# Performance work log

Measured on AMD Instinct MI355X. Metric: run time of the kernel, lower is better.

Reference implementation:

```python
import jax, jax.numpy as jnp
import numpy as np

B, S, E = 2, 2048, 2048
H, HD = 32, 64          # n_heads, head_dim
KV, REP = 8, 4          # n_kv_head, n_kv_head_rep (H == KV*REP)
NEG = -1e9


def setup_inputs() -> dict:
    key = jax.random.key(0)
    ks = jax.random.split(key, 6)
    x = jax.random.normal(ks[0], (B, S, E), dtype=jnp.float32)
    # Llama RoPE tables: angles[p, i] = p / 10000^(2i/HD)
    inv_freq = 1.0 / (10000.0 ** (jnp.arange(0, HD, 2, dtype=jnp.float32) / HD))
    angles = jnp.arange(S, dtype=jnp.float32)[:, None] * inv_freq[None, :]  # [S, HD/2]
    cos, sin = jnp.cos(angles), jnp.sin(angles)
    # causal additive mask [S, S]
    mask = jnp.where(jnp.tril(jnp.ones((S, S), dtype=bool)), 0.0, NEG).astype(jnp.float32)
    sc = 0.02
    wq = jax.random.normal(ks[1], (E, H * HD), dtype=jnp.float32) * sc
    wk = jax.random.normal(ks[2], (E, KV * HD), dtype=jnp.float32) * sc
    wv = jax.random.normal(ks[3], (E, KV * HD), dtype=jnp.float32) * sc
    wo = jax.random.normal(ks[4], (H * HD, E), dtype=jnp.float32) * sc
    return {"x": x, "cos": cos, "sin": sin, "mask": mask,
            "wq": wq, "wk": wk, "wv": wv, "wo": wo, "start_pos": 0}


def _rope(t, cos, sin):
    # t: [B, S, h, HD]; rotate consecutive pairs (Llama complex convention)
    tp = t.reshape(t.shape[:-1] + (HD // 2, 2))
    t1, t2 = tp[..., 0], tp[..., 1]
    c = cos[None, :, None, :]
    s = sin[None, :, None, :]
    out = jnp.stack([t1 * c - t2 * s, t1 * s + t2 * c], axis=-1)
    return out.reshape(t.shape)


def reference(x, cos, sin, mask, wq, wk, wv, wo, start_pos):
    b, s, _ = x.shape
    q = (x @ wq).reshape(b, s, H, HD)
    k = (x @ wk).reshape(b, s, KV, HD)
    v = (x @ wv).reshape(b, s, KV, HD)
    q = _rope(q, cos, sin)
    k = _rope(k, cos, sin)
    # KV-cache: with start_pos=0 and full-seq prefill, the cache slice
    # [:, :start_pos+s] is exactly the freshly written k/v, so use them directly.
    # Grouped attention without materializing repeated K/V:
    # q -> [b, KV, REP, s, HD]; k,v -> [b, KV, s, HD]
    qg = q.transpose(0, 2, 1, 3).reshape(b, KV, REP, s, HD)
    kg = k.transpose(0, 2, 1, 3)
    vg = v.transpose(0, 2, 1, 3)
    scale = 1.0 / jnp.sqrt(jnp.float32(HD))
    scores = jnp.einsum('bgrqd,bgkd->bgrqk', qg, kg) * scale + mask
    attn = jax.nn.softmax(scores, axis=-1)
    og = jnp.einsum('bgrqk,bgkd->bgrqd', attn, vg)     # [b, KV, REP, s, HD]
    out = og.reshape(b, H, s, HD).transpose(0, 2, 1, 3).reshape(b, s, H * HD)
    return out @ wo
```

## Files before the change

kernel.cpp:

```cpp
#include <hip/hip_runtime.h>
#include <stdint.h>

#define S_LEN 2048
#define NTOK  4096
#define EMB   2048
#define NHEAD 32
#define HDIM  64
#define NKVH  8

typedef __bf16 bf16x8 __attribute__((ext_vector_type(8)));
typedef float  f32x4  __attribute__((ext_vector_type(4)));

#define AS1 __attribute__((address_space(1)))
#define AS3 __attribute__((address_space(3)))

#if __has_builtin(__builtin_amdgcn_exp2f)
#define EXP2(x) __builtin_amdgcn_exp2f(x)
#else
#define EXP2(x) exp2f(x)
#endif

#define QSCALE 0.1803368867f

__device__ __forceinline__ uint16_t f2bf(float f) {
  uint32_t u = __float_as_uint(f);
  u += 0x7fffu + ((u >> 16) & 1u);
  return (uint16_t)(u >> 16);
}
__device__ __forceinline__ float bf2f(uint16_t h) {
  return __uint_as_float(((uint32_t)h) << 16);
}
__device__ __forceinline__ void gld16(const void* g, void* l) {
  __builtin_amdgcn_global_load_lds((const AS1 uint32_t*)g, (AS3 uint32_t*)l, 16, 0, 0);
}
__device__ __forceinline__ f32x4 mfma16(bf16x8 a, bf16x8 b, f32x4 c) {
  return __builtin_amdgcn_mfma_f32_16x16x32_bf16(a, b, c, 0, 0, 0);
}

__global__ void k_cvt(const float* __restrict__ in, uint16_t* __restrict__ out) {
  int i = (blockIdx.x * 256 + threadIdx.x) * 4;
  float4 v = *(const float4*)(in + i);
  ushort4 o;
  o.x = f2bf(v.x); o.y = f2bf(v.y); o.z = f2bf(v.z); o.w = f2bf(v.w);
  *(ushort4*)(out + i) = o;
}

__global__ void k_transpose(const float* __restrict__ in, uint16_t* __restrict__ out,
                            int R, int C) {
  __shared__ float tile[32][33];
  int c0 = blockIdx.x * 32, r0 = blockIdx.y * 32;
  int tx = threadIdx.x & 31, ty = threadIdx.x >> 5;
#pragma unroll
  for (int j = 0; j < 32; j += 8)
    tile[ty + j][tx] = in[(size_t)(r0 + ty + j) * C + c0 + tx];
  __syncthreads();
#pragma unroll
  for (int j = 0; j < 32; j += 8)
    out[(size_t)(c0 + ty + j) * R + r0 + tx] = f2bf(tile[tx][ty + j]);
}

__global__ void k_transpose_v(const uint16_t* __restrict__ qkv, uint16_t* __restrict__ out) {
  __shared__ uint16_t tile[32][33];
  int s0 = blockIdx.x * 32, hd0 = blockIdx.y * 32, bh = blockIdx.z;
  int b = bh >> 3, kvh = bh & 7;
  int tx = threadIdx.x & 31, ty = threadIdx.x >> 5;
#pragma unroll
  for (int j = 0; j < 32; j += 8)
    tile[ty + j][tx] =
        qkv[((size_t)b * S_LEN + s0 + ty + j) * 3072 + 2560 + kvh * 64 + hd0 + tx];
  __syncthreads();
#pragma unroll
  for (int j = 0; j < 32; j += 8)
    out[((size_t)bh * 64 + hd0 + ty + j) * S_LEN + s0 + tx] = tile[tx][ty + j];
}

template <int N_REP, typename OUT_T>
__global__ __launch_bounds__(512, 1) void k_gemm256(
    const uint16_t* __restrict__ A, const uint16_t* __restrict__ BT,
    OUT_T* __restrict__ C, int M, int N, int K) {
  constexpr int LDSH = 16384 + N_REP * 4096;
  __shared__ uint16_t lds[2][LDSH];
  const int tid = threadIdx.x, lane = tid & 63, w = tid >> 6;
  const int wm = w >> 2, wn = w & 3;
  const int l16 = lane & 15, lg = lane >> 4;
  const int nbn = N / (N_REP * 64);
  const int nwg = gridDim.x, cpx = nwg >> 3;
  const int swz = ((int)blockIdx.x & 7) * cpx + ((int)blockIdx.x >> 3);
  const int bm = (swz / nbn) * 256, bn = (swz % nbn) * (N_REP * 64);

  f32x4 acc[8][N_REP] = {};

  const int srow = tid >> 3, sslot = tid & 7;
  const int schunk = (sslot ^ (srow & 7)) * 8;
  const uint16_t* Ag = A + (size_t)(bm + srow) * K + schunk;
  const uint16_t* Bg = BT + (size_t)(bn + srow) * K + schunk;

  auto stageA = [&](int d, int r, int k0) {
    gld16(Ag + (size_t)r * 64 * K + k0, &lds[d][r * 4096 + tid * 8]);
  };
  auto stageB = [&](int d, int r, int k0) {
    gld16(Bg + (size_t)r * 64 * K + k0, &lds[d][16384 + r * 4096 + tid * 8]);
  };
  auto lda = [&](int d, int mf, int s) -> bf16x8 {
    int row = wm * 128 + mf * 16 + l16;
    int slot = (s * 4 + lg) ^ (row & 7);
    return *(const bf16x8*)(&lds[d][row * 64 + slot * 8]);
  };
  auto ldb = [&](int d, int nf, int s) -> bf16x8 {
    int row = wn * (N_REP * 16) + nf * 16 + l16;
    int slot = (s * 4 + lg) ^ (row & 7);
    return *(const bf16x8*)(&lds[d][16384 + row * 64 + slot * 8]);
  };

  const int NT = K >> 6;
#pragma unroll
  for (int r = 0; r < 4; ++r) stageA(0, r, 0);
#pragma unroll
  for (int r = 0; r < N_REP; ++r) stageB(0, r, 0);
#pragma unroll
  for (int r = 0; r < 4; ++r) if (1 < NT) stageA(1, r, 64);
  asm volatile("s_waitcnt vmcnt(4)" ::: "memory");
  __builtin_amdgcn_s_barrier();

  for (int kt = 0; kt < NT; ++kt) {
    const int cur = kt & 1;
    const int nk0 = (kt + 1) << 6, nnk0 = (kt + 2) << 6;
    const bool m1 = (kt + 1 < NT), m2 = (kt + 2 < NT);
    bf16x8 a[4][2], a2[4][2], b[N_REP][2];
#pragma unroll
    for (int mi = 0; mi < 4; ++mi) { a[mi][0] = lda(cur, mi, 0); a[mi][1] = lda(cur, mi, 1); }
#pragma unroll
    for (int ni = 0; ni < N_REP; ++ni) { b[ni][0] = ldb(cur, ni, 0); b[ni][1] = ldb(cur, ni, 1); }
    if (m1) {
#pragma unroll
      for (int r = 0; r < N_REP; ++r) stageB(cur ^ 1, r, nk0);
    }
    __builtin_amdgcn_s_barrier();
    asm volatile("s_waitcnt lgkmcnt(0)" ::: "memory");
    __builtin_amdgcn_sched_barrier(0);
    __builtin_amdgcn_s_setprio(1);
#pragma unroll
    for (int mi = 0; mi < 4; ++mi)
#pragma unroll
      for (int ni = 0; ni < 2; ++ni) {
        acc[mi][ni] = mfma16(a[mi][0], b[ni][0], acc[mi][ni]);
        acc[mi][ni] = mfma16(a[mi][1], b[ni][1], acc[mi][ni]);
      }
    __builtin_amdgcn_s_setprio(0);
    __builtin_amdgcn_s_barrier();
#pragma unroll
    for (int mi = 0; mi < 4; ++mi) { a2[mi][0] = lda(cur, 4 + mi, 0); a2[mi][1] = lda(cur, 4 + mi, 1); }
    __builtin_amdgcn_s_barrier();
    asm volatile("s_waitcnt lgkmcnt(0)" ::: "memory");
    __builtin_amdgcn_sched_barrier(0);
    __builtin_amdgcn_s_setprio(1);
    if constexpr (N_REP == 3) {
#pragma unroll
      for (int mi = 0; mi < 4; ++mi) {
        acc[mi][2] = mfma16(a[mi][0], b[2][0], acc[mi][2]);
        acc[mi][2] = mfma16(a[mi][1], b[2][1], acc[mi][2]);
      }
    }
#pragma unroll
    for (int mi = 0; mi < 4; ++mi) {
      acc[4 + mi][0] = mfma16(a2[mi][0], b[0][0], acc[4 + mi][0]);
      acc[4 + mi][0] = mfma16(a2[mi][1], b[0][1], acc[4 + mi][0]);
    }
    __builtin_amdgcn_s_setprio(0);
    __builtin_amdgcn_s_barrier();
    if (m2) {
#pragma unroll
      for (int r = 0; r < 4; ++r) stageA(cur, r, nnk0);
    }
    __builtin_amdgcn_s_setprio(1);
#pragma unroll
    for (int mi = 0; mi < 4; ++mi)
#pragma unroll
      for (int ni = 1; ni < N_REP; ++ni) {
        acc[4 + mi][ni] = mfma16(a2[mi][0], b[ni][0], acc[4 + mi][ni]);
        acc[4 + mi][ni] = mfma16(a2[mi][1], b[ni][1], acc[4 + mi][ni]);
      }
    __builtin_amdgcn_s_setprio(0);
    if (m2) { asm volatile("s_waitcnt vmcnt(4)" ::: "memory"); }
    else    { asm volatile("s_waitcnt vmcnt(0)" ::: "memory"); }
    __builtin_amdgcn_s_barrier();
  }
#pragma unroll
  for (int mf = 0; mf < 8; ++mf)
#pragma unroll
    for (int nf = 0; nf < N_REP; ++nf)
#pragma unroll
      for (int r = 0; r < 4; ++r) {
        int row = bm + wm * 128 + mf * 16 + lg * 4 + r;
        int col = bn + wn * (N_REP * 16) + nf * 16 + l16;
        float v = acc[mf][nf][r];
        if constexpr (sizeof(OUT_T) == 4) C[(size_t)row * N + col] = v;
        else                              C[(size_t)row * N + col] = f2bf(v);
      }
}

__global__ void k_rope(const uint16_t* __restrict__ qkv, const float* __restrict__ cosT,
                       const float* __restrict__ sinT, uint16_t* __restrict__ qb,
                       uint16_t* __restrict__ kb) {
  int idx = blockIdx.x * 256 + threadIdx.x;
  int row = idx / 1280;
  int col = (idx - row * 1280) * 2;
  int s = row & (S_LEN - 1);
  uint32_t vv = *(const uint32_t*)(qkv + (size_t)row * 3072 + col);
  float t1 = bf2f((uint16_t)vv), t2 = bf2f((uint16_t)(vv >> 16));
  int i = (col & 63) >> 1;
  if (col < 2048) {
    float c = cosT[s * 32 + i] * QSCALE, sn = sinT[s * 32 + i] * QSCALE;
    uint32_t o = (uint32_t)f2bf(t1 * c - t2 * sn) | ((uint32_t)f2bf(t1 * sn + t2 * c) << 16);
    *(uint32_t*)(qb + (size_t)row * 2048 + col) = o;
  } else {
    int cc = col - 2048;
    float c = cosT[s * 32 + i], sn = sinT[s * 32 + i];
    uint32_t o = (uint32_t)f2bf(t1 * c - t2 * sn) | ((uint32_t)f2bf(t1 * sn + t2 * c) << 16);
    *(uint32_t*)(kb + (size_t)row * 512 + cc) = o;
  }
}

template <bool MASKED>
__device__ __forceinline__ void tile_compute(
    const uint16_t* Kc, const uint16_t* Vc, const bf16x8 qf[2][2], bf16x8 onesv,
    int l16, int lg, int kv0, int qb0,
    float m_r[2], f32x4 lacc[2], f32x4 acc[2][4]) {
  f32x4 st[2][4] = {};
  __builtin_amdgcn_s_setprio(1);
#pragma unroll
  for (int c = 0; c < 4; ++c) {
    int row = c * 16 + l16, sw = row & 7;
    bf16x8 ka  = *(const bf16x8*)(Kc + row * 64 + ((lg ^ sw) * 8));
    bf16x8 kb2 = *(const bf16x8*)(Kc + row * 64 + (((4 | lg) ^ sw) * 8));
#pragma unroll
    for (int qc = 0; qc < 2; ++qc) {
      st[qc][c] = mfma16(ka,  qf[qc][0], st[qc][c]);
      st[qc][c] = mfma16(kb2, qf[qc][1], st[qc][c]);
    }
  }
  __builtin_amdgcn_s_setprio(0);
  bf16x8 pu[2][2];
#pragma unroll
  for (int qc = 0; qc < 2; ++qc) {
    const int qrow = qb0 + qc * 16 + l16;
    float sv[4][4];
#pragma unroll
    for (int c = 0; c < 4; ++c)
#pragma unroll
      for (int r = 0; r < 4; ++r) {
        float s = st[qc][c][r];
        if (MASKED && (kv0 + c * 16 + lg * 4 + r > qrow)) s = -1e30f;
        sv[c][r] = s;
      }
    float m0 = fmaxf(fmaxf(sv[0][0], sv[0][1]), fmaxf(sv[0][2], sv[0][3]));
    float m1 = fmaxf(fmaxf(sv[1][0], sv[1][1]), fmaxf(sv[1][2], sv[1][3]));
    float m2 = fmaxf(fmaxf(sv[2][0], sv[2][1]), fmaxf(sv[2][2], sv[2][3]));
    float m3 = fmaxf(fmaxf(sv[3][0], sv[3][1]), fmaxf(sv[3][2], sv[3][3]));
    float mx = fmaxf(fmaxf(m0, m1), fmaxf(m2, m3));
    mx = fmaxf(mx, __shfl_xor(mx, 16));
    mx = fmaxf(mx, __shfl_xor(mx, 32));
    if (!__all(mx - m_r[qc] <= 8.0f)) {
      float m_new = fmaxf(m_r[qc], mx);
      float alpha = EXP2(m_r[qc] - m_new);
      float al[4];
#pragma unroll
      for (int r = 0; r < 4; ++r) al[r] = __shfl(alpha, lg * 4 + r);
#pragma unroll
      for (int n = 0; n < 4; ++n)
#pragma unroll
        for (int r = 0; r < 4; ++r) acc[qc][n][r] *= al[r];
#pragma unroll
      for (int r = 0; r < 4; ++r) lacc[qc][r] *= al[r];
      m_r[qc] = m_new;
    }
    float pf[4][4];
#pragma unroll
    for (int c = 0; c < 4; ++c)
#pragma unroll
      for (int r = 0; r < 4; ++r)
        pf[c][r] = EXP2(sv[c][r] - m_r[qc]);
#pragma unroll
    for (int cc = 0; cc < 2; ++cc)
#pragma unroll
      for (int e = 0; e < 8; ++e)
        ((__bf16*)&pu[qc][cc])[e] = (__bf16)pf[cc * 2 + (e >> 2)][e & 3];
  }
  __builtin_amdgcn_s_setprio(1);
#pragma unroll
  for (int cc = 0; cc < 2; ++cc) {
    lacc[0] = mfma16(pu[0][cc], onesv, lacc[0]);
    lacc[1] = mfma16(pu[1][cc], onesv, lacc[1]);
#pragma unroll
    for (int n = 0; n < 4; ++n) {
      int row = n * 16 + l16, sw2 = row & 7;
      int k0 = cc * 32 + lg * 4, k1 = k0 + 16;
      const char* base = (const char*)Vc + row * 128;
      union { uint64_t q[2]; bf16x8 v; } vu;
      vu.q[0] = *(const uint64_t*)(base + (((k0 >> 3) ^ sw2) << 4) + ((k0 & 7) << 1));
      vu.q[1] = *(const uint64_t*)(base + (((k1 >> 3) ^ sw2) << 4) + ((k1 & 7) << 1));
      acc[0][n] = mfma16(pu[0][cc], vu.v, acc[0][n]);
      acc[1][n] = mfma16(pu[1][cc], vu.v, acc[1][n]);
    }
  }
  __builtin_amdgcn_s_setprio(0);
}

__global__ __launch_bounds__(256, 4) void k_flash(
    const uint16_t* __restrict__ Qb, const uint16_t* __restrict__ Kb,
    const uint16_t* __restrict__ VT, uint16_t* __restrict__ Ob) {
  __shared__ uint16_t Ks[2][4096];
  __shared__ uint16_t Vs[2][4096];
  const int j = 63 - ((int)blockIdx.x >> 4);
  const int gb = blockIdx.x & 15;
  const int g = gb & 7, b = gb >> 3;
  const int tid = threadIdx.x, lane = tid & 63, w = tid >> 6;
  const int l16 = lane & 15, lg = lane >> 4;
  const int h = g * 4 + w;
  const int qb0 = j * 32;

  bf16x8 qf[2][2];
#pragma unroll
  for (int qc = 0; qc < 2; ++qc) {
    const size_t tokq = (size_t)b * S_LEN + qb0 + qc * 16 + l16;
    qf[qc][0] = *(const bf16x8*)(Qb + tokq * 2048 + h * 64 + lg * 8);
    qf[qc][1] = *(const bf16x8*)(Qb + tokq * 2048 + h * 64 + 32 + lg * 8);
  }
  bf16x8 onesv;
#pragma unroll
  for (int e = 0; e < 8; ++e) ((__bf16*)&onesv)[e] = (__bf16)1.0f;

  const int srow = tid >> 3, shc = tid & 7;
  const int swz = (shc ^ (srow & 7)) * 8;
  const uint16_t* Kg = Kb + ((size_t)b * S_LEN + srow) * 512 + g * 64 + swz;
  const uint16_t* Vg = VT + ((size_t)(b * 8 + g) * 64 + srow) * S_LEN + swz;

  float m_r[2] = {-1e30f, -1e30f};
  f32x4 lacc[2] = {};
  f32x4 acc[2][4] = {};
  const int nt = (j >> 1) + 1;

  auto stage = [&](int t, int buf) {
    const size_t kv0 = (size_t)t * 64;
    uint16_t* kd = &Ks[buf][tid * 8];
    uint16_t* vd = &Vs[buf][tid * 8];
    gld16(Kg + kv0 * 512, kd);
    gld16(Kg + (kv0 + 32) * 512, kd + 2048);
    gld16(Vg + kv0, vd);
    gld16(Vg + kv0 + (size_t)32 * S_LEN, vd + 2048);
  };

  stage(0, 0);

  for (int t = 0; t < nt; ++t) {
    const int cur = t & 1;
    asm volatile("s_waitcnt vmcnt(0)" ::: "memory");
    __builtin_amdgcn_s_barrier();
    if (t + 1 < nt) stage(t + 1, cur ^ 1);
    if (t == nt - 1)
      tile_compute<true >(Ks[cur], Vs[cur], qf, onesv, l16, lg, t * 64, qb0, m_r, lacc, acc);
    else
      tile_compute<false>(Ks[cur], Vs[cur], qf, onesv, l16, lg, t * 64, qb0, m_r, lacc, acc);
  }
#pragma unroll
  for (int qc = 0; qc < 2; ++qc) {
    float li[4];
#pragma unroll
    for (int r = 0; r < 4; ++r) li[r] = 1.0f / lacc[qc][r];
#pragma unroll
    for (int n = 0; n < 4; ++n)
#pragma unroll
      for (int r = 0; r < 4; ++r) {
        int qo = qb0 + qc * 16 + lg * 4 + r;
        Ob[((size_t)b * S_LEN + qo) * 2048 + h * 64 + n * 16 + l16] =
            f2bf(acc[qc][n][r] * li[r]);
      }
  }
}

extern "C" void kernel_launch(void* const* d_in, const int* in_sizes, int n_in,
                              void* d_out, int out_size, void* d_ws, size_t ws_size,
                              hipStream_t stream) {
  const float* x    = (const float*)d_in[0];
  const float* cosT = (const float*)d_in[1];
  const float* sinT = (const float*)d_in[2];
  const float* wq   = (const float*)d_in[4];
  const float* wk   = (const float*)d_in[5];
  const float* wv   = (const float*)d_in[6];
  const float* wo   = (const float*)d_in[7];
  float* out = (float*)d_out;

  char* ws = (char*)d_ws;
  size_t off = 0;
  auto alloc = [&](size_t bytes) {
    void* p = ws + off;
    off += (bytes + 255) & ~(size_t)255;
    return p;
  };
  uint16_t* xb   = (uint16_t*)alloc((size_t)NTOK * EMB * 2);
  uint16_t* wT   = (uint16_t*)alloc((size_t)3072 * 2048 * 2);
  uint16_t* woT  = (uint16_t*)alloc((size_t)2048 * 2048 * 2);
  uint16_t* qkvb = (uint16_t*)alloc((size_t)NTOK * 3072 * 2);
  uint16_t* qb   = (uint16_t*)alloc((size_t)NTOK * 2048 * 2);
  uint16_t* kb   = (uint16_t*)alloc((size_t)NTOK * 512 * 2);
  uint16_t* vT   = (uint16_t*)alloc((size_t)NTOK * 512 * 2);
  uint16_t* ob   = xb;

  k_cvt<<<(NTOK * EMB) / 1024, 256, 0, stream>>>(x, xb);
  k_transpose<<<dim3(64, 64), 256, 0, stream>>>(wq, wT, 2048, 2048);
  k_transpose<<<dim3(16, 64), 256, 0, stream>>>(wk, wT + (size_t)2048 * 2048, 2048, 512);
  k_transpose<<<dim3(16, 64), 256, 0, stream>>>(wv, wT + (size_t)2560 * 2048, 2048, 512);
  k_transpose<<<dim3(64, 64), 256, 0, stream>>>(wo, woT, 2048, 2048);

  k_gemm256<3, uint16_t><<<256, 512, 0, stream>>>(xb, wT, qkvb, 4096, 3072, 2048);
  k_rope<<<(NTOK * 1280) / 256, 256, 0, stream>>>(qkvb, cosT, sinT, qb, kb);
  k_transpose_v<<<dim3(64, 2, 16), 256, 0, stream>>>(qkvb, vT);
  k_flash<<<dim3(1024), 256, 0, stream>>>(qb, kb, vT, ob);
  k_gemm256<2, float><<<256, 512, 0, stream>>>(ob, woT, out, 4096, 2048, 2048);
}
```

Baseline: 185.4 us.

## Add 128x128 GEMM for output projection and compute softmax row sums with shuffles

Adds a new 256-thread, 128x128-tile bf16 MFMA GEMM kernel and uses it for the output projection with 512 workgroups instead of 256. In the flash kernel, the softmax denominator was accumulated with an MFMA against a ones vector; it is now a scalar per-row sum reduced with lane shuffles, which removes two MFMAs per tile. The flash kernel's launch-bounds occupancy hint drops from 4 to 3. The new GEMM may reuse less data per tile than the 256-tile version, and the lower occupancy hint could help or hurt flash.

```diff
diff --git a/kernel.cpp b/kernel.cpp
--- a/kernel.cpp
+++ b/kernel.cpp
@@ -193,6 +193,125 @@
       for (int r = 0; r < 4; ++r) {
         int row = bm + wm * 128 + mf * 16 + lg * 4 + r;
         int col = bn + wn * (N_REP * 16) + nf * 16 + l16;
+        float v = acc[mf][nf][r];
+        if constexpr (sizeof(OUT_T) == 4) C[(size_t)row * N + col] = v;
+        else                              C[(size_t)row * N + col] = f2bf(v);
+      }
+}
+
+template <typename OUT_T>
+__global__ __launch_bounds__(256, 2) void k_gemm128(
+    const uint16_t* __restrict__ A, const uint16_t* __restrict__ BT,
+    OUT_T* __restrict__ C, int M, int N, int K) {
+  __shared__ uint16_t lds[2][16384];
+  const int tid = threadIdx.x, lane = tid & 63, w = tid >> 6;
+  const int wm = w >> 1, wn = w & 1;
+  const int l16 = lane & 15, lg = lane >> 4;
+  const int nbn = N >> 7;
+  const int nwg = gridDim.x, cpx = nwg >> 3;
+  const int swz = ((int)blockIdx.x & 7) * cpx + ((int)blockIdx.x >> 3);
+  const int bm = (swz / nbn) * 128, bn = (swz % nbn) * 128;
+
+  f32x4 acc[4][4] = {};
+
+  const int srow = tid >> 3, sslot = tid & 7;
+  const int schunk = (sslot ^ (srow & 7)) * 8;
+  const uint16_t* Ag = A + (size_t)(bm + srow) * K + schunk;
+  const uint16_t* Bg = BT + (size_t)(bn + srow) * K + schunk;
+
+  auto stageA = [&](int d, int r, int k0) {
+    gld16(Ag + (size_t)r * 32 * K + k0, &lds[d][r * 2048 + tid * 8]);
+  };
+  auto stageB = [&](int d, int r, int k0) {
+    gld16(Bg + (size_t)r * 32 * K + k0, &lds[d][8192 + r * 2048 + tid * 8]);
+  };
+  auto lda = [&](int d, int mf, int s) -> bf16x8 {
+    int row = wm * 64 + mf * 16 + l16;
+    int slot = (s * 4 + lg) ^ (row & 7);
+    return *(const bf16x8*)(&lds[d][row * 64 + slot * 8]);
+  };
+  auto ldb = [&](int d, int nf, int s) -> bf16x8 {
+    int row = wn * 64 + nf * 16 + l16;
+    int slot = (s * 4 + lg) ^ (row & 7);
+    return *(const bf16x8*)(&lds[d][8192 + row * 64 + slot * 8]);
+  };
+
+  const int NT = K >> 6;
+#pragma unroll
+  for (int r = 0; r < 4; ++r) stageA(0, r, 0);
+#pragma unroll
+  for (int r = 0; r < 4; ++r) stageB(0, r, 0);
+#pragma unroll
+  for (int r = 0; r < 4; ++r) if (1 < NT) stageA(1, r, 64);
+  asm volatile("s_waitcnt vmcnt(4)" ::: "memory");
+  __builtin_amdgcn_s_barrier();
+
+  for (int kt = 0; kt < NT; ++kt) {
+    const int cur = kt & 1;
+    const int nk0 = (kt + 1) << 6, nnk0 = (kt + 2) << 6;
+    const bool m1 = (kt + 1 < NT), m2 = (kt + 2 < NT);
+    bf16x8 a[2][2], a2[2][2], b[4][2];
+#pragma unroll
+    for (int mi = 0; mi < 2; ++mi) { a[mi][0] = lda(cur, mi, 0); a[mi][1] = lda(cur, mi, 1); }
+#pragma unroll
+    for (int ni = 0; ni < 4; ++ni) { b[ni][0] = ldb(cur, ni, 0); b[ni][1] = ldb(cur, ni, 1); }
+    if (m1) {
+#pragma unroll
+      for (int r = 0; r < 4; ++r) stageB(cur ^ 1, r, nk0);
+    }
+    __builtin_amdgcn_s_barrier();
+    asm volatile("s_waitcnt lgkmcnt(0)" ::: "memory");
+    __builtin_amdgcn_sched_barrier(0);
+    __builtin_amdgcn_s_setprio(1);
+#pragma unroll
+    for (int mi = 0; mi < 2; ++mi)
+#pragma unroll
+      for (int ni = 0; ni < 4; ++ni) {
+        acc[mi][ni] = mfma16(a[mi][0], b[ni][0], acc[mi][ni]);
+        acc[mi][ni] = mfma16(a[mi][1], b[ni][1], acc[mi][ni]);
+      }
+    __builtin_amdgcn_s_setprio(0);
+    __builtin_amdgcn_s_barrier();
+#pragma unroll
+    for (int mi = 0; mi < 2; ++mi) { a2[mi][0] = lda(cur, 2 + mi, 0); a2[mi][1] = lda(cur, 2 + mi, 1); }
+    __builtin_amdgcn_s_barrier();
+    asm volatile("s_waitcnt lgkmcnt(0)" ::: "memory");
+    __builtin_amdgcn_sched_barrier(0);
+    __builtin_amdgcn_s_setprio(1);
+#pragma unroll
+    for (int mi = 0; mi < 2; ++mi)
+#pragma unroll
+      for (int ni = 0; ni < 2; ++ni) {
+        acc[2 + mi][ni] = mfma16(a2[mi][0], b[ni][0], acc[2 + mi][ni]);
+        acc[2 + mi][ni] = mfma16(a2[mi][1], b[ni][1], acc[2 + mi][ni]);
+      }
+    __builtin_amdgcn_s_setprio(0);
+    __builtin_amdgcn_s_barrier();
+    if (m2) {
+#pragma unroll
+      for (int r = 0; r < 4; ++r) stageA(cur, r, nnk0);
+    }
+    __builtin_amdgcn_s_setprio(1);
+#pragma unroll
+    for (int mi = 0; mi < 2; ++mi)
+#pragma unroll
+      for (int ni = 2; ni < 4; ++ni) {
+        acc[2 + mi][ni] = mfma16(a2[mi][0], b[ni][0], acc[2 + mi][ni]);
+        acc[2 + mi][ni] = mfma16(a2[mi][1], b[ni][1], acc[2 + mi][ni]);
+      }
+    __builtin_amdgcn_s_setprio(0);
+    if (m2) { asm volatile("s_waitcnt vmcnt(4)" ::: "memory"); }
+    else    { asm volatile("s_waitcnt vmcnt(0)" ::: "memory"); }
+    __builtin_amdgcn_s_barrier();
+  }
+#pragma unroll
+  for (int mf = 0; mf < 4; ++mf)
+#pragma unroll
+    for (int nf = 0; nf < 4; ++nf)
+#pragma unroll
+      for (int r = 0; r < 4; ++r) {
+        int row = bm + wm * 64 + mf * 16 + lg * 4 + r;
+        int col = bn + wn * 64 + nf * 16 + l16;
         float v = acc[mf][nf][r];
         if constexpr (sizeof(OUT_T) == 4) C[(size_t)row * N + col] = v;
         else                              C[(size_t)row * N + col] = f2bf(v);
@@ -223,9 +342,9 @@
 
 template <bool MASKED>
 __device__ __forceinline__ void tile_compute(
-    const uint16_t* Kc, const uint16_t* Vc, const bf16x8 qf[2][2], bf16x8 onesv,
+    const uint16_t* Kc, const uint16_t* Vc, const bf16x8 qf[2][2],
     int l16, int lg, int kv0, int qb0,
-    float m_r[2], f32x4 lacc[2], f32x4 acc[2][4]) {
+    float m_r[2], float l_r[2], f32x4 acc[2][4]) {
   f32x4 st[2][4] = {};
   __builtin_amdgcn_s_setprio(1);
 #pragma unroll
@@ -270,8 +389,7 @@
       for (int n = 0; n < 4; ++n)
 #pragma unroll
         for (int r = 0; r < 4; ++r) acc[qc][n][r] *= al[r];
-#pragma unroll
-      for (int r = 0; r < 4; ++r) lacc[qc][r] *= al[r];
+      l_r[qc] *= alpha;
       m_r[qc] = m_new;
     }
     float pf[4][4];
@@ -280,6 +398,13 @@
 #pragma unroll
       for (int r = 0; r < 4; ++r)
         pf[c][r] = EXP2(sv[c][r] - m_r[qc]);
+    float ps = 0.f;
+#pragma unroll
+    for (int c = 0; c < 4; ++c)
+      ps += (pf[c][0] + pf[c][1]) + (pf[c][2] + pf[c][3]);
+    ps += __shfl_xor(ps, 16);
+    ps += __shfl_xor(ps, 32);
+    l_r[qc] += ps;
 #pragma unroll
     for (int cc = 0; cc < 2; ++cc)
 #pragma unroll
@@ -289,8 +414,6 @@
   __builtin_amdgcn_s_setprio(1);
 #pragma unroll
   for (int cc = 0; cc < 2; ++cc) {
-    lacc[0] = mfma16(pu[0][cc], onesv, lacc[0]);
-    lacc[1] = mfma16(pu[1][cc], onesv, lacc[1]);
 #pragma unroll
     for (int n = 0; n < 4; ++n) {
       int row = n * 16 + l16, sw2 = row & 7;
@@ -306,7 +429,7 @@
   __builtin_amdgcn_s_setprio(0);
 }
 
-__global__ __launch_bounds__(256, 4) void k_flash(
+__global__ __launch_bounds__(256, 3) void k_flash(
     const uint16_t* __restrict__ Qb, const uint16_t* __restrict__ Kb,
     const uint16_t* __restrict__ VT, uint16_t* __restrict__ Ob) {
   __shared__ uint16_t Ks[2][4096];
@@ -326,9 +449,6 @@
     qf[qc][0] = *(const bf16x8*)(Qb + tokq * 2048 + h * 64 + lg * 8);
     qf[qc][1] = *(const bf16x8*)(Qb + tokq * 2048 + h * 64 + 32 + lg * 8);
   }
-  bf16x8 onesv;
-#pragma unroll
-  for (int e = 0; e < 8; ++e) ((__bf16*)&onesv)[e] = (__bf16)1.0f;
 
   const int srow = tid >> 3, shc = tid & 7;
   const int swz = (shc ^ (srow & 7)) * 8;
@@ -336,7 +456,7 @@
   const uint16_t* Vg = VT + ((size_t)(b * 8 + g) * 64 + srow) * S_LEN + swz;
 
   float m_r[2] = {-1e30f, -1e30f};
-  f32x4 lacc[2] = {};
+  float l_r[2] = {0.f, 0.f};
   f32x4 acc[2][4] = {};
   const int nt = (j >> 1) + 1;
 
@@ -358,15 +478,15 @@
     __builtin_amdgcn_s_barrier();
     if (t + 1 < nt) stage(t + 1, cur ^ 1);
     if (t == nt - 1)
-      tile_compute<true >(Ks[cur], Vs[cur], qf, onesv, l16, lg, t * 64, qb0, m_r, lacc, acc);
+      tile_compute<true >(Ks[cur], Vs[cur], qf, l16, lg, t * 64, qb0, m_r, l_r, acc);
     else
-      tile_compute<false>(Ks[cur], Vs[cur], qf, onesv, l16, lg, t * 64, qb0, m_r, lacc, acc);
+      tile_compute<false>(Ks[cur], Vs[cur], qf, l16, lg, t * 64, qb0, m_r, l_r, acc);
   }
 #pragma unroll
   for (int qc = 0; qc < 2; ++qc) {
     float li[4];
 #pragma unroll
-    for (int r = 0; r < 4; ++r) li[r] = 1.0f / lacc[qc][r];
+    for (int r = 0; r < 4; ++r) li[r] = 1.0f / __shfl(l_r[qc], lg * 4 + r);
 #pragma unroll
     for (int n = 0; n < 4; ++n)
 #pragma unroll
@@ -416,5 +536,5 @@
   k_rope<<<(NTOK * 1280) / 256, 256, 0, stream>>>(qkvb, cosT, sinT, qb, kb);
   k_transpose_v<<<dim3(64, 2, 16), 256, 0, stream>>>(qkvb, vT);
   k_flash<<<dim3(1024), 256, 0, stream>>>(qb, kb, vT, ob);
-  k_gemm256<2, float><<<256, 512, 0, stream>>>(ob, woT, out, 4096, 2048, 2048);
-}
+  k_gemm128<float><<<512, 256, 0, stream>>>(ob, woT, out, 4096, 2048, 2048);
+}
```

New measurement: 185.6 us. Within noise of the previous version (+0.1%).
